# Performance work log

Measured on AMD Instinct MI355X. Metric: run time of the kernel, lower is better.

## Reference

```python
import jax, jax.numpy as jnp
import numpy as np

B, N, D_PATCH = 32, 196, 768
TKN, QK, H, HID = 768, 64, 12, 3072
K_STEPS = 12
ALPHA = 1.0
BETA = 1.0 / (QK ** 0.5)
EPS = 1e-5


def setup_inputs() -> dict:
    key = jax.random.key(0)
    ks = jax.random.split(key, 8)
    w_std = 0.002
    return {
        "x": jax.random.normal(ks[0], (B, N, D_PATCH), jnp.float32),
        "w_enc": jax.random.normal(ks[1], (TKN, D_PATCH), jnp.float32) * 0.02,
        "b_enc": jnp.zeros((TKN,), jnp.float32),
        "cls_tok": jnp.ones((1, 1, TKN), jnp.float32),
        "pos": jax.random.normal(ks[2], (1, N + 1, TKN), jnp.float32) * w_std,
        "eln_gamma": jnp.ones((1,), jnp.float32),
        "eln_bias": jnp.zeros((TKN,), jnp.float32),
        "wq": jax.random.normal(ks[3], (H, QK, TKN), jnp.float32) * w_std,
        "wk": jax.random.normal(ks[4], (H, QK, TKN), jnp.float32) * w_std,
        "w_hop": jax.random.normal(ks[5], (HID, TKN), jnp.float32) * 0.02,
        "dec_ln_w": jnp.ones((TKN,), jnp.float32),
        "dec_ln_b": jnp.zeros((TKN,), jnp.float32),
        "w_dec": jax.random.normal(ks[6], (D_PATCH, TKN), jnp.float32) * 0.02,
        "b_dec": jnp.zeros((D_PATCH,), jnp.float32),
    }


def _energy(g, wq, wk, w_hop):
    # attention energy: non-softmax, -1/beta * sum logsumexp(beta * A)
    q = jnp.einsum('bnd,hzd->bnhz', g, wq)
    k = jnp.einsum('bnd,hzd->bnhz', g, wk)
    A = jnp.einsum('bqhz,bkhz->bhqk', q, k)  # [B,H,N+1,N+1]
    e_attn = (-1.0 / BETA) * jnp.sum(jax.nn.logsumexp(BETA * A, axis=-1))
    # Hopfield energy: -0.5 * sum relu(g W^T)^2
    h = jnp.einsum('bnd,fd->bnf', g, w_hop)  # [B,N+1,HID]
    e_hop = -0.5 * jnp.sum(jax.nn.relu(h) ** 2)
    return e_attn + e_hop


def _energy_ln(x, gamma, bias):
    xm = x - x.mean(-1, keepdims=True)
    o = xm / jnp.sqrt((xm ** 2).mean(-1, keepdims=True) + EPS)
    return gamma * o + bias


def _layernorm(x, w, b):
    mu = x.mean(-1, keepdims=True)
    xm = x - mu
    var = (xm ** 2).mean(-1, keepdims=True)
    return xm / jnp.sqrt(var + EPS) * w + b


def reference(x, w_enc, b_enc, cls_tok, pos, eln_gamma, eln_bias,
              wq, wk, w_hop, dec_ln_w, dec_ln_b, w_dec, b_dec):
    # encode: Linear(d_patch -> tkn)
    t = jnp.einsum('bnd,td->bnt', x, w_enc) + b_enc
    # prepend cls, add positional encoding
    cls = jnp.broadcast_to(cls_tok, (t.shape[0], 1, TKN))
    t = jnp.concatenate([cls, t], axis=1) + pos  # [B, N+1, TKN]

    grad_e = jax.grad(lambda g: _energy(g, wq, wk, w_hop))
    for _ in range(K_STEPS):  # fixed unroll over time steps (single block)
        g = _energy_ln(t, eln_gamma, eln_bias)
        t = t - ALPHA * grad_e(g)

    # decode: LayerNorm + Linear(tkn -> d_patch)
    y = _layernorm(t, dec_ln_w, dec_ln_b)
    y = jnp.einsum('bnt,dt->bnd', y, w_dec) + b_dec
    return y[:, 1:]  # drop cls token (use_cls=False)
```

## Files before the change

kernel.cpp:

```cpp
#include <hip/hip_runtime.h>
#include <hip/hip_bf16.h>

typedef __hip_bfloat16 bf16;
typedef short s8 __attribute__((ext_vector_type(8)));
typedef short sv4 __attribute__((ext_vector_type(4)));
typedef float f4 __attribute__((ext_vector_type(4)));

#define BETA 0.125f
#define EPS 1e-5f

__device__ __forceinline__ void gld16(const void* g, void* l){
    __builtin_amdgcn_global_load_lds(
        (const __attribute__((address_space(1))) void*)g,
        (__attribute__((address_space(3))) void*)l, 16, 0, 0);
}

__global__ __launch_bounds__(256) void f2b_k(const float* __restrict__ in, bf16* __restrict__ out, long n){
    long i = (long)blockIdx.x*256 + threadIdx.x;
    if (i < n) out[i] = __float2bfloat16(in[i]);
}
__global__ __launch_bounds__(256) void padx_k(const float* __restrict__ x, bf16* __restrict__ xb){
    long i = (long)blockIdx.x*256 + threadIdx.x;
    if (i >= 6400L*768) return;
    long row = i / 768;
    xb[i] = (row < 6272) ? __float2bfloat16(x[i]) : __float2bfloat16(0.f);
}
__global__ __launch_bounds__(256) void tr_k(const short* __restrict__ Bi, short* __restrict__ Bo){
    __shared__ short t[32][33];
    int i0 = blockIdx.x*32, j0 = blockIdx.y*32;
    int li = threadIdx.x & 31, lj = threadIdx.x >> 5;
    #pragma unroll
    for (int r=0;r<4;r++) t[lj+8*r][li] = Bi[(long)(i0+lj+8*r)*768 + j0+li];
    __syncthreads();
    #pragma unroll
    for (int r=0;r<4;r++) Bo[(long)(j0+lj+8*r)*4608 + i0+li] = t[li][lj+8*r];
}

__global__ __launch_bounds__(256) void cls_k(const float* __restrict__ cls, const float* __restrict__ pos,
                                             float* __restrict__ t){
    int i = blockIdx.x*256 + threadIdx.x;
    int b = i / 768, c = i % 768;
    t[((long)b*197)*768 + c] = cls[c] + pos[c];
}

template<int MODE>
__global__ __launch_bounds__(256) void big_gemm(
    const short* __restrict__ A, int lda,
    const short* __restrict__ B, int ldb,
    float* __restrict__ Cf, bf16* __restrict__ Cb, int ldc,
    int K, int Nn, int Nm, int relu0, long zoff,
    const float* __restrict__ bias, const float* __restrict__ pos)
{
    const int f = blockIdx.x;
    const int npg = 16*Nn;
    const int grp = f / npg;
    const int first_m = grp*16;
    const int gs = (Nm - first_m < 16) ? (Nm - first_m) : 16;
    const int rem = f % npg;
    const int bm = first_m + rem % gs;
    const int bn = rem / gs;

    __shared__ short lsA[8192];
    __shared__ short lsB[8192];
    const int tid = threadIdx.x;
    const int w = tid>>6, l = tid&63;
    const int m0 = bm*128, n0 = bn*128;
    const int srow = tid>>2;
    const int qglob = ((tid&3) - (tid>>3)) & 3;
    const int scol = qglob*8;
    int koff, Ks;
    if (MODE==1){ Ks = K>>1; koff = blockIdx.z * Ks; Cf += (size_t)blockIdx.z * zoff; }
    else        { Ks = K;    koff = 0; }
    const short* pa = A + (size_t)(m0+srow)*lda + koff + scol;
    const short* pb = B + (size_t)(n0+srow)*ldb + koff + scol;
    short* laP = lsA + w*512;
    short* lbP = lsB + w*512;
    const int wm = (w>>1)*64, wn = (w&1)*64;
    const int fr = l&15, fq = ((l>>4) + (fr>>1) & 3)*8;
    f4 acc[4][4] = {};
    const int nk = Ks>>6;
    for (int kt=0; kt<nk; kt++){
        const size_t ko = (size_t)kt*64;
        const size_t ra = 64*(size_t)lda, rb = 64*(size_t)ldb;
        gld16(pa + ko,           laP);
        gld16(pa + ko + ra,      laP + 2048);
        gld16(pa + ko + 32,      laP + 4096);
        gld16(pa + ko + 32 + ra, laP + 6144);
        gld16(pb + ko,           lbP);
        gld16(pb + ko + rb,      lbP + 2048);
        gld16(pb + ko + 32,      lbP + 4096);
        gld16(pb + ko + 32 + rb, lbP + 6144);
        __syncthreads();
        #pragma unroll
        for (int ks=0; ks<2; ks++){
            s8 af[4], bfr[4];
            #pragma unroll
            for (int i=0;i<4;i++) af[i]  = *(const s8*)(lsA + ks*4096 + (wm+i*16+fr)*32 + fq);
            #pragma unroll
            for (int j=0;j<4;j++) bfr[j] = *(const s8*)(lsB + ks*4096 + (wn+j*16+fr)*32 + fq);
            #pragma unroll
            for (int i=0;i<4;i++)
                #pragma unroll
                for (int j=0;j<4;j++)
                    acc[i][j] = __builtin_amdgcn_mfma_f32_16x16x32_bf16(af[i], bfr[j], acc[i][j], 0,0,0);
        }
        __syncthreads();
    }
    const int er = (l>>4)*4;
    const int ec = l&15;
    #pragma unroll
    for (int i=0;i<4;i++){
        #pragma unroll
        for (int j=0;j<4;j++){
            int gr0 = m0 + wm + i*16 + er;
            int gc  = n0 + wn + j*16 + ec;
            #pragma unroll
            for (int r=0;r<4;r++){
                float v = acc[i][j][r];
                int gr = gr0 + r;
                if (MODE==0){
                    if (gc >= relu0) v = v>0.f ? v : 0.f;
                    Cb[(size_t)gr*ldc + gc] = __float2bfloat16(v);
                } else if (MODE==1){
                    Cf[(size_t)gr*ldc + gc] = v;
                } else if (MODE==2){
                    if (gr < 6272){
                        int b = gr/196, n = gr%196;
                        Cf[((size_t)b*197 + n + 1)*768 + gc] = v + bias[gc] + pos[(long)(n+1)*768+gc];
                    }
                } else {
                    if (gr < 6272) Cf[(size_t)gr*ldc + gc] = v + bias[gc];
                }
            }
        }
    }
}

__global__ __launch_bounds__(256) void pack_k(const short* __restrict__ qkh,
                                              short* __restrict__ qT, short* __restrict__ kT){
    __shared__ short tq[64][65];
    __shared__ short tk[64][65];
    const int bh = blockIdx.x, b = bh/12, h = bh%12;
    const int mc = blockIdx.y*64;
    const int tid = threadIdx.x;
    #pragma unroll
    for (int e=0;e<16;e++){
        int i = tid + e*256; int r = i>>6, c = i&63;
        int mg = mc + r;
        short vq = 0, vk = 0;
        if (mg < 197){
            size_t base = (size_t)(b*197+mg)*4608 + h*64 + c;
            vq = qkh[base]; vk = qkh[base+768];
        }
        tq[r][c] = vq; tk[r][c] = vk;
    }
    __syncthreads();
    #pragma unroll
    for (int e=0;e<16;e++){
        int i = tid + e*256; int zr = i>>6, cm = i&63;
        size_t o = (size_t)bh*16384 + (size_t)zr*256 + mc + cm;
        qT[o] = tq[cm][zr];
        kT[o] = tk[cm][zr];
    }
}

__global__ __launch_bounds__(256) void attn_k(
    short* __restrict__ qkh, const short* __restrict__ qT, const short* __restrict__ kT)
{
    __shared__ short Pl[64*232];
    __shared__ short Ptl[208*72];
    const int bh = blockIdx.x, b = bh/12, h = bh%12;
    const int tid = threadIdx.x, w = tid>>6, l = tid&63;
    const int lr = l&15, lq = l>>4;
    const size_t qcol = (size_t)h*64, kcol = 768 + qcol;
    const size_t rbase = (size_t)b*197*4608;
    const short* qTp = qT + (size_t)bh*16384;
    const short* kTp = kT + (size_t)bh*16384;

    for (int i=tid; i<64*16; i+=256){ int r=i>>4, c=208+(i&15); Pl[r*232+c]=0; }

    f4 ak[13];
    #pragma unroll
    for (int t=0;t<13;t++) ak[t] = (f4){0.f,0.f,0.f,0.f};

    for (int iter=0; iter<4; iter++){
        const int m0 = iter*64;
        f4 S[13];
        #pragma unroll
        for (int t=0;t<13;t++) S[t] = (f4){0.f,0.f,0.f,0.f};
        const int mrow = m0 + w*16 + lr;
        #pragma unroll
        for (int ks=0; ks<2; ks++){
            s8 af = *(const s8*)(qkh + rbase + (size_t)mrow*4608 + qcol + ks*32 + lq*8);
            #pragma unroll
            for (int t=0;t<13;t++){
                s8 bf = *(const s8*)(qkh + rbase + (size_t)(t*16+lr)*4608 + kcol + ks*32 + lq*8);
                S[t] = __builtin_amdgcn_mfma_f32_16x16x32_bf16(af, bf, S[t], 0,0,0);
            }
        }
        __syncthreads();
        const int mbase = w*16 + lq*4;
        #pragma unroll
        for (int r=0;r<4;r++){
            float mx = -1e30f;
            #pragma unroll
            for (int t=0;t<13;t++){
                float v = S[t][r]*BETA;
                if (t==12 && lr>=5) v = -1e30f;
                S[t][r] = v;
                mx = fmaxf(mx, v);
            }
            mx = fmaxf(mx, __shfl_xor(mx,1,64)); mx = fmaxf(mx, __shfl_xor(mx,2,64));
            mx = fmaxf(mx, __shfl_xor(mx,4,64)); mx = fmaxf(mx, __shfl_xor(mx,8,64));
            float sm = 0.f;
            #pragma unroll
            for (int t=0;t<13;t++){ float e = __expf(S[t][r]-mx); S[t][r]=e; sm+=e; }
            sm += __shfl_xor(sm,1,64); sm += __shfl_xor(sm,2,64);
            sm += __shfl_xor(sm,4,64); sm += __shfl_xor(sm,8,64);
            float inv = 1.f/sm;
            bool valid = (m0 + mbase + r) < 197;
            #pragma unroll
            for (int t=0;t<13;t++) S[t][r] = valid ? S[t][r]*inv : 0.f;
        }
        #pragma unroll
        for (int t=0;t<13;t++){
            int c = t*16 + lr;
            short pb[4];
            #pragma unroll
            for (int r=0;r<4;r++){
                bf16 bv = __float2bfloat16(S[t][r]);
                pb[r] = *(short*)&bv;
                Pl[(mbase+r)*232 + c] = pb[r];
            }
            *(sv4*)(Ptl + c*72 + mbase) = (sv4){pb[0],pb[1],pb[2],pb[3]};
        }
        __syncthreads();
        f4 aq[4];
        #pragma unroll
        for (int t=0;t<4;t++) aq[t] = (f4){0.f,0.f,0.f,0.f};
        #pragma unroll
        for (int ks=0; ks<7; ks++){
            s8 af = *(const s8*)(kTp + (w*16+lr)*256 + ks*32 + lq*8);
            #pragma unroll
            for (int mt=0;mt<4;mt++){
                s8 bf = *(const s8*)(Pl + (mt*16+lr)*232 + ks*32 + lq*8);
                aq[mt] = __builtin_amdgcn_mfma_f32_16x16x32_bf16(af, bf, aq[mt], 0,0,0);
            }
        }
        #pragma unroll
        for (int mt=0;mt<4;mt++){
            int mg = m0 + mt*16 + lr;
            if (mg < 197){
                sv4 pv;
                #pragma unroll
                for (int r=0;r<4;r++){ bf16 bv=__float2bfloat16(aq[mt][r]); pv[r]=*(short*)&bv; }
                *(sv4*)(qkh + rbase + (size_t)mg*4608 + qcol + w*16 + lq*4) = pv;
            }
        }
        #pragma unroll
        for (int ks=0; ks<2; ks++){
            s8 bf = *(const s8*)(qTp + (w*16+lr)*256 + m0 + ks*32 + lq*8);
            #pragma unroll
            for (int t=0;t<13;t++){
                s8 af = *(const s8*)(Ptl + (t*16+lr)*72 + ks*32 + lq*8);
                ak[t] = __builtin_amdgcn_mfma_f32_16x16x32_bf16(af, bf, ak[t], 0,0,0);
            }
        }
    }
    #pragma unroll
    for (int t=0;t<13;t++){
        #pragma unroll
        for (int r=0;r<4;r++){
            int n = t*16 + lq*4 + r;
            if (n < 197)
                *(bf16*)(qkh + rbase + (size_t)n*4608 + kcol + w*16 + lr) = __float2bfloat16(ak[t][r]);
        }
    }
}

__global__ __launch_bounds__(256) void ln_k(
    float* __restrict__ in, bf16* __restrict__ out,
    const float* __restrict__ p0, const float* __restrict__ p1,
    const float* __restrict__ scale, const float* __restrict__ bias,
    int scalar_scale, int rowmap, int addp, int writet)
{
    int r = blockIdx.x;
    long src = rowmap ? ((long)(r/196)*197 + r%196 + 1) : (long)r;
    float* xr = in + src*768;
    int tid = threadIdx.x;
    float v0 = xr[tid], v1 = xr[tid+256], v2 = xr[tid+512];
    if (addp){
        const float* a = p0 + src*768;
        const float* b = p1 + src*768;
        v0 += a[tid]     + b[tid];
        v1 += a[tid+256] + b[tid+256];
        v2 += a[tid+512] + b[tid+512];
        if (writet){ xr[tid]=v0; xr[tid+256]=v1; xr[tid+512]=v2; }
    }
    __shared__ float red[4];
    float s = v0+v1+v2;
    #pragma unroll
    for (int o=1;o<64;o<<=1) s += __shfl_xor(s, o, 64);
    if ((tid&63)==0) red[tid>>6] = s;
    __syncthreads();
    float mu = (red[0]+red[1]+red[2]+red[3]) * (1.f/768.f);
    float d0=v0-mu, d1=v1-mu, d2=v2-mu;
    float q = d0*d0 + d1*d1 + d2*d2;
    #pragma unroll
    for (int o=1;o<64;o<<=1) q += __shfl_xor(q, o, 64);
    __syncthreads();
    if ((tid&63)==0) red[tid>>6] = q;
    __syncthreads();
    float ms = (red[0]+red[1]+red[2]+red[3]) * (1.f/768.f);
    float inv = rsqrtf(ms + EPS);
    bf16* o_ = out + (long)r*768;
    float s0 = scalar_scale ? scale[0] : scale[tid];
    float s1 = scalar_scale ? s0 : scale[tid+256];
    float s2 = scalar_scale ? s0 : scale[tid+512];
    o_[tid]     = __float2bfloat16(d0*inv*s0 + bias[tid]);
    o_[tid+256] = __float2bfloat16(d1*inv*s1 + bias[tid+256]);
    o_[tid+512] = __float2bfloat16(d2*inv*s2 + bias[tid+512]);
}

extern "C" void kernel_launch(void* const* d_in, const int* in_sizes, int n_in,
                              void* d_out, int out_size, void* d_ws, size_t ws_size,
                              hipStream_t stream) {
    const float* x       = (const float*)d_in[0];
    const float* w_enc   = (const float*)d_in[1];
    const float* b_enc   = (const float*)d_in[2];
    const float* cls_tok = (const float*)d_in[3];
    const float* pos     = (const float*)d_in[4];
    const float* eln_g   = (const float*)d_in[5];
    const float* eln_b   = (const float*)d_in[6];
    const float* wq      = (const float*)d_in[7];
    const float* wk      = (const float*)d_in[8];
    const float* w_hop   = (const float*)d_in[9];
    const float* dln_w   = (const float*)d_in[10];
    const float* dln_b   = (const float*)d_in[11];
    const float* w_dec   = (const float*)d_in[12];
    const float* b_dec   = (const float*)d_in[13];
    float* out = (float*)d_out;

    float* t_  = (float*)d_ws;
    bf16* g_   = (bf16*)(t_ + 6400L*768);
    bf16* qkh  = g_ + 6400L*768;
    bf16* qT   = qkh + 6400L*4608;
    bf16* kT   = qT + 384L*16384;
    float* p0  = (float*)(kT + 384L*16384);
    float* p1  = p0 + 6400L*768;
    bf16* B1   = (bf16*)(p1 + 6400L*768);
    bf16* B2   = B1 + 4608L*768;
    bf16* we_  = B2 + 768L*4608;
    bf16* wd_  = we_ + 768L*768;

    dim3 blk(256);
    const long ZOFF = 6400L*768;

    f2b_k<<<dim3((589824+255)/256),  blk, 0, stream>>>(wq,    B1,          589824);
    f2b_k<<<dim3((589824+255)/256),  blk, 0, stream>>>(wk,    B1+589824,   589824);
    f2b_k<<<dim3((2359296+255)/256), blk, 0, stream>>>(w_hop, B1+1179648, 2359296);
    f2b_k<<<dim3((589824+255)/256),  blk, 0, stream>>>(w_enc, we_,         589824);
    f2b_k<<<dim3((589824+255)/256),  blk, 0, stream>>>(w_dec, wd_,         589824);
    tr_k<<<dim3(144,24), blk, 0, stream>>>((const short*)B1, (short*)B2);
    padx_k<<<dim3((int)((6400L*768+255)/256)), blk, 0, stream>>>(x, g_);

    cls_k<<<dim3(96), blk, 0, stream>>>(cls_tok, pos, t_);
    big_gemm<2><<<dim3(300), blk, 0, stream>>>((const short*)g_, 768, (const short*)we_, 768,
                                               t_, nullptr, 768, 768, 6, 50, 0, 0, b_enc, pos);

    for (int step=0; step<12; step++){
        ln_k<<<dim3(6304), blk, 0, stream>>>(t_, g_, p0, p1, eln_g, eln_b, 1, 0, step>0, 1);
        big_gemm<0><<<dim3(1800), blk, 0, stream>>>((const short*)g_, 768, (const short*)B1, 768,
                                                    nullptr, qkh, 4608, 768, 36, 50, 1536, 0, nullptr, nullptr);
        pack_k<<<dim3(384,4), blk, 0, stream>>>((const short*)qkh, (short*)qT, (short*)kT);
        attn_k<<<dim3(384), blk, 0, stream>>>((short*)qkh, (const short*)qT, (const short*)kT);
        big_gemm<1><<<dim3(300,1,2), blk, 0, stream>>>((const short*)qkh, 4608, (const short*)B2, 4608,
                                                       p0, nullptr, 768, 4608, 6, 50, 0, ZOFF, nullptr, nullptr);
    }

    ln_k<<<dim3(6272), blk, 0, stream>>>(t_, g_, p0, p1, dln_w, dln_b, 0, 1, 1, 0);
    big_gemm<3><<<dim3(300), blk, 0, stream>>>((const short*)g_, 768, (const short*)wd_, 768,
                                               out, nullptr, 768, 768, 6, 50, 0, 0, b_dec, nullptr);
}
```

Measured before the change: 2.638 ms.

## Double-buffer GEMM LDS loads, fuse pack into attention, vectorize LN, merge conversions

```diff
diff --git a/kernel.cpp b/kernel.cpp
--- a/kernel.cpp
+++ b/kernel.cpp
@@ -15,16 +15,28 @@
         (__attribute__((address_space(3))) void*)l, 16, 0, 0);
 }
 
-__global__ __launch_bounds__(256) void f2b_k(const float* __restrict__ in, bf16* __restrict__ out, long n){
+__global__ __launch_bounds__(256) void cvt_k(
+    const float* __restrict__ wq, const float* __restrict__ wk, const float* __restrict__ whop,
+    const float* __restrict__ wenc, const float* __restrict__ wdec, const float* __restrict__ x,
+    bf16* __restrict__ B1, bf16* __restrict__ we, bf16* __restrict__ wd, bf16* __restrict__ xb)
+{
     long i = (long)blockIdx.x*256 + threadIdx.x;
-    if (i < n) out[i] = __float2bfloat16(in[i]);
-}
-__global__ __launch_bounds__(256) void padx_k(const float* __restrict__ x, bf16* __restrict__ xb){
-    long i = (long)blockIdx.x*256 + threadIdx.x;
-    if (i >= 6400L*768) return;
-    long row = i / 768;
-    xb[i] = (row < 6272) ? __float2bfloat16(x[i]) : __float2bfloat16(0.f);
-}
+    if (i < 3538944){
+        const float* s; long j = i;
+        if (j < 589824) s = wq;
+        else if (j < 1179648){ s = wk; j -= 589824; }
+        else { s = whop; j -= 1179648; }
+        B1[i] = __float2bfloat16(s[j]);
+    } else if (i < 4128768){
+        long j = i - 3538944; we[j] = __float2bfloat16(wenc[j]);
+    } else if (i < 4718592){
+        long j = i - 4128768; wd[j] = __float2bfloat16(wdec[j]);
+    } else if (i < 9633792){
+        long j = i - 4718592; long row = j / 768;
+        xb[j] = (row < 6272) ? __float2bfloat16(x[j]) : __float2bfloat16(0.f);
+    }
+}
+
 __global__ __launch_bounds__(256) void tr_k(const short* __restrict__ Bi, short* __restrict__ Bo){
     __shared__ short t[32][33];
     int i0 = blockIdx.x*32, j0 = blockIdx.y*32;
@@ -73,39 +85,41 @@
     else        { Ks = K;    koff = 0; }
     const short* pa = A + (size_t)(m0+srow)*lda + koff + scol;
     const short* pb = B + (size_t)(n0+srow)*ldb + koff + scol;
-    short* laP = lsA + w*512;
-    short* lbP = lsB + w*512;
+    const size_t ra = 64*(size_t)lda, rb = 64*(size_t)ldb;
     const int wm = (w>>1)*64, wn = (w&1)*64;
     const int fr = l&15, fq = ((l>>4) + (fr>>1) & 3)*8;
     f4 acc[4][4] = {};
-    const int nk = Ks>>6;
-    for (int kt=0; kt<nk; kt++){
-        const size_t ko = (size_t)kt*64;
-        const size_t ra = 64*(size_t)lda, rb = 64*(size_t)ldb;
-        gld16(pa + ko,           laP);
-        gld16(pa + ko + ra,      laP + 2048);
-        gld16(pa + ko + 32,      laP + 4096);
-        gld16(pa + ko + 32 + ra, laP + 6144);
-        gld16(pb + ko,           lbP);
-        gld16(pb + ko + rb,      lbP + 2048);
-        gld16(pb + ko + 32,      lbP + 4096);
-        gld16(pb + ko + 32 + rb, lbP + 6144);
-        __syncthreads();
-        #pragma unroll
-        for (int ks=0; ks<2; ks++){
-            s8 af[4], bfr[4];
-            #pragma unroll
-            for (int i=0;i<4;i++) af[i]  = *(const s8*)(lsA + ks*4096 + (wm+i*16+fr)*32 + fq);
-            #pragma unroll
-            for (int j=0;j<4;j++) bfr[j] = *(const s8*)(lsB + ks*4096 + (wn+j*16+fr)*32 + fq);
-            #pragma unroll
-            for (int i=0;i<4;i++)
-                #pragma unroll
-                for (int j=0;j<4;j++)
-                    acc[i][j] = __builtin_amdgcn_mfma_f32_16x16x32_bf16(af[i], bfr[j], acc[i][j], 0,0,0);
-        }
-        __syncthreads();
-    }
+    const int nk = Ks>>5;
+
+    gld16(pa,      lsA + w*512);
+    gld16(pa + ra, lsA + 2048 + w*512);
+    gld16(pb,      lsB + w*512);
+    gld16(pb + rb, lsB + 2048 + w*512);
+
+    #pragma unroll 2
+    for (int p=0; p<nk; p++){
+        const int half = p & 1;
+        __syncthreads();
+        if (p+1 < nk){
+            const int h2 = (p+1) & 1;
+            const size_t ko = (size_t)(p+1)*32;
+            gld16(pa + ko,      lsA + h2*4096 + w*512);
+            gld16(pa + ko + ra, lsA + h2*4096 + 2048 + w*512);
+            gld16(pb + ko,      lsB + h2*4096 + w*512);
+            gld16(pb + ko + rb, lsB + h2*4096 + 2048 + w*512);
+        }
+        s8 af[4], bfr[4];
+        #pragma unroll
+        for (int i=0;i<4;i++) af[i]  = *(const s8*)(lsA + half*4096 + (wm+i*16+fr)*32 + fq);
+        #pragma unroll
+        for (int j=0;j<4;j++) bfr[j] = *(const s8*)(lsB + half*4096 + (wn+j*16+fr)*32 + fq);
+        #pragma unroll
+        for (int i=0;i<4;i++)
+            #pragma unroll
+            for (int j=0;j<4;j++)
+                acc[i][j] = __builtin_amdgcn_mfma_f32_16x16x32_bf16(af[i], bfr[j], acc[i][j], 0,0,0);
+    }
+
     const int er = (l>>4)*4;
     const int ec = l&15;
     #pragma unroll
@@ -136,47 +150,43 @@
     }
 }
 
-__global__ __launch_bounds__(256) void pack_k(const short* __restrict__ qkh,
-                                              short* __restrict__ qT, short* __restrict__ kT){
-    __shared__ short tq[64][65];
-    __shared__ short tk[64][65];
-    const int bh = blockIdx.x, b = bh/12, h = bh%12;
-    const int mc = blockIdx.y*64;
-    const int tid = threadIdx.x;
-    #pragma unroll
-    for (int e=0;e<16;e++){
-        int i = tid + e*256; int r = i>>6, c = i&63;
-        int mg = mc + r;
-        short vq = 0, vk = 0;
-        if (mg < 197){
-            size_t base = (size_t)(b*197+mg)*4608 + h*64 + c;
-            vq = qkh[base]; vk = qkh[base+768];
-        }
-        tq[r][c] = vq; tk[r][c] = vk;
-    }
-    __syncthreads();
-    #pragma unroll
-    for (int e=0;e<16;e++){
-        int i = tid + e*256; int zr = i>>6, cm = i&63;
-        size_t o = (size_t)bh*16384 + (size_t)zr*256 + mc + cm;
-        qT[o] = tq[cm][zr];
-        kT[o] = tk[cm][zr];
-    }
-}
-
-__global__ __launch_bounds__(256) void attn_k(
-    short* __restrict__ qkh, const short* __restrict__ qT, const short* __restrict__ kT)
+__global__ __launch_bounds__(256) void attn_k(short* __restrict__ qkh)
 {
-    __shared__ short Pl[64*232];
-    __shared__ short Ptl[208*72];
+    __shared__ short sm[65664];
+    short* qTl = sm;
+    short* kTl = sm + 17920;
+    short* Pl  = sm + 35840;
+    short* Ptl = sm + 50688;
+    short* tq  = sm + 35840;
+    short* tk  = sm + 40000;
+
     const int bh = blockIdx.x, b = bh/12, h = bh%12;
     const int tid = threadIdx.x, w = tid>>6, l = tid&63;
     const int lr = l&15, lq = l>>4;
     const size_t qcol = (size_t)h*64, kcol = 768 + qcol;
     const size_t rbase = (size_t)b*197*4608;
-    const short* qTp = qT + (size_t)bh*16384;
-    const short* kTp = kT + (size_t)bh*16384;
-
+
+    for (int mc=0; mc<256; mc+=64){
+        #pragma unroll
+        for (int e=0;e<16;e++){
+            int i = tid + e*256; int r = i>>6, c = i&63;
+            int mg = mc + r;
+            short vq = 0, vk = 0;
+            if (mg < 197){
+                size_t base = rbase + (size_t)mg*4608 + qcol + c;
+                vq = qkh[base]; vk = qkh[base+768];
+            }
+            tq[r*65+c] = vq; tk[r*65+c] = vk;
+        }
+        __syncthreads();
+        #pragma unroll
+        for (int e=0;e<16;e++){
+            int i = tid + e*256; int zr = i>>6, cm = i&63;
+            qTl[zr*280 + mc + cm] = tq[cm*65+zr];
+            kTl[zr*280 + mc + cm] = tk[cm*65+zr];
+        }
+        __syncthreads();
+    }
     for (int i=tid; i<64*16; i+=256){ int r=i>>4, c=208+(i&15); Pl[r*232+c]=0; }
 
     f4 ak[13];
@@ -212,12 +222,12 @@
             }
             mx = fmaxf(mx, __shfl_xor(mx,1,64)); mx = fmaxf(mx, __shfl_xor(mx,2,64));
             mx = fmaxf(mx, __shfl_xor(mx,4,64)); mx = fmaxf(mx, __shfl_xor(mx,8,64));
-            float sm = 0.f;
-            #pragma unroll
-            for (int t=0;t<13;t++){ float e = __expf(S[t][r]-mx); S[t][r]=e; sm+=e; }
-            sm += __shfl_xor(sm,1,64); sm += __shfl_xor(sm,2,64);
-            sm += __shfl_xor(sm,4,64); sm += __shfl_xor(sm,8,64);
-            float inv = 1.f/sm;
+            float sm_ = 0.f;
+            #pragma unroll
+            for (int t=0;t<13;t++){ float e = __expf(S[t][r]-mx); S[t][r]=e; sm_+=e; }
+            sm_ += __shfl_xor(sm_,1,64); sm_ += __shfl_xor(sm_,2,64);
+            sm_ += __shfl_xor(sm_,4,64); sm_ += __shfl_xor(sm_,8,64);
+            float inv = 1.f/sm_;
             bool valid = (m0 + mbase + r) < 197;
             #pragma unroll
             for (int t=0;t<13;t++) S[t][r] = valid ? S[t][r]*inv : 0.f;
@@ -240,7 +250,7 @@
         for (int t=0;t<4;t++) aq[t] = (f4){0.f,0.f,0.f,0.f};
         #pragma unroll
         for (int ks=0; ks<7; ks++){
-            s8 af = *(const s8*)(kTp + (w*16+lr)*256 + ks*32 + lq*8);
+            s8 af = *(const s8*)(kTl + (w*16+lr)*280 + ks*32 + lq*8);
             #pragma unroll
             for (int mt=0;mt<4;mt++){
                 s8 bf = *(const s8*)(Pl + (mt*16+lr)*232 + ks*32 + lq*8);
@@ -259,7 +269,7 @@
         }
         #pragma unroll
         for (int ks=0; ks<2; ks++){
-            s8 bf = *(const s8*)(qTp + (w*16+lr)*256 + m0 + ks*32 + lq*8);
+            s8 bf = *(const s8*)(qTl + (w*16+lr)*280 + m0 + ks*32 + lq*8);
             #pragma unroll
             for (int t=0;t<13;t++){
                 s8 af = *(const s8*)(Ptl + (t*16+lr)*72 + ks*32 + lq*8);
@@ -286,26 +296,28 @@
 {
     int r = blockIdx.x;
     long src = rowmap ? ((long)(r/196)*197 + r%196 + 1) : (long)r;
-    float* xr = in + src*768;
+    float4* xr = (float4*)(in + src*768);
     int tid = threadIdx.x;
-    float v0 = xr[tid], v1 = xr[tid+256], v2 = xr[tid+512];
-    if (addp){
-        const float* a = p0 + src*768;
-        const float* b = p1 + src*768;
-        v0 += a[tid]     + b[tid];
-        v1 += a[tid+256] + b[tid+256];
-        v2 += a[tid+512] + b[tid+512];
-        if (writet){ xr[tid]=v0; xr[tid+256]=v1; xr[tid+512]=v2; }
+    float4 v = {0.f,0.f,0.f,0.f};
+    if (tid < 192){
+        v = xr[tid];
+        if (addp){
+            float4 a = ((const float4*)(p0 + src*768))[tid];
+            float4 b = ((const float4*)(p1 + src*768))[tid];
+            v.x += a.x+b.x; v.y += a.y+b.y; v.z += a.z+b.z; v.w += a.w+b.w;
+            if (writet) xr[tid] = v;
+        }
     }
     __shared__ float red[4];
-    float s = v0+v1+v2;
+    float s = v.x+v.y+v.z+v.w;
     #pragma unroll
     for (int o=1;o<64;o<<=1) s += __shfl_xor(s, o, 64);
     if ((tid&63)==0) red[tid>>6] = s;
     __syncthreads();
     float mu = (red[0]+red[1]+red[2]+red[3]) * (1.f/768.f);
-    float d0=v0-mu, d1=v1-mu, d2=v2-mu;
-    float q = d0*d0 + d1*d1 + d2*d2;
+    float d0=v.x-mu, d1=v.y-mu, d2=v.z-mu, d3=v.w-mu;
+    float q = d0*d0 + d1*d1 + d2*d2 + d3*d3;
+    if (tid >= 192) q = 0.f;
     #pragma unroll
     for (int o=1;o<64;o<<=1) q += __shfl_xor(q, o, 64);
     __syncthreads();
@@ -313,13 +325,19 @@
     __syncthreads();
     float ms = (red[0]+red[1]+red[2]+red[3]) * (1.f/768.f);
     float inv = rsqrtf(ms + EPS);
-    bf16* o_ = out + (long)r*768;
-    float s0 = scalar_scale ? scale[0] : scale[tid];
-    float s1 = scalar_scale ? s0 : scale[tid+256];
-    float s2 = scalar_scale ? s0 : scale[tid+512];
-    o_[tid]     = __float2bfloat16(d0*inv*s0 + bias[tid]);
-    o_[tid+256] = __float2bfloat16(d1*inv*s1 + bias[tid+256]);
-    o_[tid+512] = __float2bfloat16(d2*inv*s2 + bias[tid+512]);
+    if (tid < 192){
+        int c = tid*4;
+        float s0 = scalar_scale ? scale[0] : scale[c];
+        float s1 = scalar_scale ? s0 : scale[c+1];
+        float s2 = scalar_scale ? s0 : scale[c+2];
+        float s3 = scalar_scale ? s0 : scale[c+3];
+        bf16 b0 = __float2bfloat16(d0*inv*s0 + bias[c]);
+        bf16 b1 = __float2bfloat16(d1*inv*s1 + bias[c+1]);
+        bf16 b2 = __float2bfloat16(d2*inv*s2 + bias[c+2]);
+        bf16 b3 = __float2bfloat16(d3*inv*s3 + bias[c+3]);
+        sv4 pv = { *(short*)&b0, *(short*)&b1, *(short*)&b2, *(short*)&b3 };
+        ((sv4*)(out + (long)r*768))[tid] = pv;
+    }
 }
 
 extern "C" void kernel_launch(void* const* d_in, const int* in_sizes, int n_in,
@@ -344,9 +362,7 @@
     float* t_  = (float*)d_ws;
     bf16* g_   = (bf16*)(t_ + 6400L*768);
     bf16* qkh  = g_ + 6400L*768;
-    bf16* qT   = qkh + 6400L*4608;
-    bf16* kT   = qT + 384L*16384;
-    float* p0  = (float*)(kT + 384L*16384);
+    float* p0  = (float*)(qkh + 6400L*4608);
     float* p1  = p0 + 6400L*768;
     bf16* B1   = (bf16*)(p1 + 6400L*768);
     bf16* B2   = B1 + 4608L*768;
@@ -356,13 +372,9 @@
     dim3 blk(256);
     const long ZOFF = 6400L*768;
 
-    f2b_k<<<dim3((589824+255)/256),  blk, 0, stream>>>(wq,    B1,          589824);
-    f2b_k<<<dim3((589824+255)/256),  blk, 0, stream>>>(wk,    B1+589824,   589824);
-    f2b_k<<<dim3((2359296+255)/256), blk, 0, stream>>>(w_hop, B1+1179648, 2359296);
-    f2b_k<<<dim3((589824+255)/256),  blk, 0, stream>>>(w_enc, we_,         589824);
-    f2b_k<<<dim3((589824+255)/256),  blk, 0, stream>>>(w_dec, wd_,         589824);
+    cvt_k<<<dim3(37632), blk, 0, stream>>>(wq, wk, w_hop, w_enc, w_dec, x,
+                                           B1, we_, wd_, g_);
     tr_k<<<dim3(144,24), blk, 0, stream>>>((const short*)B1, (short*)B2);
-    padx_k<<<dim3((int)((6400L*768+255)/256)), blk, 0, stream>>>(x, g_);
 
     cls_k<<<dim3(96), blk, 0, stream>>>(cls_tok, pos, t_);
     big_gemm<2><<<dim3(300), blk, 0, stream>>>((const short*)g_, 768, (const short*)we_, 768,
@@ -372,8 +384,7 @@
         ln_k<<<dim3(6304), blk, 0, stream>>>(t_, g_, p0, p1, eln_g, eln_b, 1, 0, step>0, 1);
         big_gemm<0><<<dim3(1800), blk, 0, stream>>>((const short*)g_, 768, (const short*)B1, 768,
                                                     nullptr, qkh, 4608, 768, 36, 50, 1536, 0, nullptr, nullptr);
-        pack_k<<<dim3(384,4), blk, 0, stream>>>((const short*)qkh, (short*)qT, (short*)kT);
-        attn_k<<<dim3(384), blk, 0, stream>>>((short*)qkh, (const short*)qT, (const short*)kT);
+        attn_k<<<dim3(384), blk, 0, stream>>>((short*)qkh);
         big_gemm<1><<<dim3(300,1,2), blk, 0, stream>>>((const short*)qkh, 4608, (const short*)B2, 4608,
                                                        p0, nullptr, 768, 4608, 6, 50, 0, ZOFF, nullptr, nullptr);
     }
```

Result: slower. 2.749 ms (+4.2%).
